# Performance work log

Hardware: AMD Instinct MI355X
Metric: run time of the kernel (lower is better)

Reference implementation:

```python
import jax, jax.numpy as jnp
import numpy as np
from jax import lax

P = 0.1  # WTA keep fraction (mode='per_image')


def setup_inputs() -> dict:
    key = jax.random.key(0)
    x = jax.random.normal(key, (32, 256, 64, 64), dtype=jnp.float32)
    return {"x": x}


def reference(x) -> jnp.ndarray:
    bs, nc, sz, _ = x.shape
    k = int(np.ceil(nc * sz * sz * P))  # 104858 for these shapes
    flat = x.reshape(bs, -1)                      # [bs, nc*sz*sz]
    topk_vals = lax.top_k(flat, k)[0]             # [bs, k], descending
    thr = topk_vals[:, -1].reshape(bs, 1, 1, 1)   # k-th largest per image
    return x * (x >= thr).astype(x.dtype)
```

## Files before the change

### kernel.cpp

```cpp
#include <hip/hip_runtime.h>
#include <hip/hip_bf16.h>
#include <stdint.h>


#define IMGS    32
#define NPER    1048576
#define NPER4   (NPER / 4)
#define NBINS   8192
#define BPI_H   32
#define BPI_M   64
#define CAP     16384
#define LCAP    2048
#define CSTRIDE 64

__device__ __forceinline__ unsigned mapf(float f) {
    unsigned u = __float_as_uint(f);
    return (u & 0x80000000u) ? ~u : (u | 0x80000000u);
}

__device__ __forceinline__ void block_scan256(unsigned* p, int t, unsigned v) {
    p[t] = v;
    __syncthreads();
    #pragma unroll
    for (int off = 1; off < 256; off <<= 1) {
        unsigned u = (t >= off) ? p[t - off] : 0u;
        __syncthreads();
        p[t] += u;
        __syncthreads();
    }
}

__global__ void k_zero(uint4* __restrict__ p, int n16) {
    int i = blockIdx.x * blockDim.x + threadIdx.x;
    if (i < n16) p[i] = make_uint4(0u, 0u, 0u, 0u);
}

__global__ void k_hist(const float4* __restrict__ x4, unsigned* __restrict__ hist) {
    __shared__ unsigned h[NBINS];
    int t = threadIdx.x;
    for (int j = t; j < NBINS; j += 256) h[j] = 0u;
    __syncthreads();

    int bx = blockIdx.x;
    int img = bx >> 5;
    long long base4 = (long long)img * NPER4 + (long long)(bx & 31) * 8192;
    for (int it = 0; it < 32; ++it) {
        float4 v = x4[base4 + it * 256 + t];
        atomicAdd(&h[mapf(v.x) >> 19], 1u);
        atomicAdd(&h[mapf(v.y) >> 19], 1u);
        atomicAdd(&h[mapf(v.z) >> 19], 1u);
        atomicAdd(&h[mapf(v.w) >> 19], 1u);
    }
    __syncthreads();

    unsigned* gh = hist + (long long)img * NBINS;
    for (int j = t; j < NBINS; j += 256) {
        unsigned c = h[j];
        if (c) atomicAdd(&gh[j], c);
    }
}

__global__ void k_scan(const unsigned* __restrict__ hist, uint2* __restrict__ binfo,
                       unsigned k) {
    int img = blockIdx.x;
    const unsigned* h = hist + (long long)img * NBINS;
    __shared__ unsigned bins[NBINS];
    __shared__ unsigned pre[256];
    int t = threadIdx.x;

    for (int idx = t; idx < NBINS; idx += 256) bins[idx] = h[idx];
    __syncthreads();

    unsigned s = 0;
    #pragma unroll
    for (int j = 0; j < 32; ++j) s += bins[t * 32 + ((j + t) & 31)];

    block_scan256(pre, t, s);
    unsigned total_above = pre[255] - pre[t];
    if (total_above < k && total_above + s >= k) {
        unsigned cum = total_above;
        for (int j = 31; j >= 0; --j) {
            unsigned v = bins[t * 32 + j];
            cum += v;
            if (cum >= k) {
                binfo[img] = make_uint2((unsigned)(t * 32 + j), k - (cum - v));
                break;
            }
        }
    }
}

__global__ void k_mask(const float4* __restrict__ x4, float4* __restrict__ o4,
                       const uint2* __restrict__ binfo, unsigned* __restrict__ counters,
                       unsigned* __restrict__ candKey, unsigned* __restrict__ candIdx) {
    __shared__ unsigned lkey[LCAP];
    __shared__ unsigned lidx[LCAP];
    __shared__ unsigned lcnt;
    __shared__ unsigned gbase;
    int t = threadIdx.x;
    if (t == 0) lcnt = 0u;
    __syncthreads();

    int bx = blockIdx.x;
    int img = bx >> 6;
    unsigned b13 = binfo[img].x;
    long long base4 = (long long)img * NPER4 + (long long)(bx & 63) * 4096;

    for (int it = 0; it < 16; ++it) {
        long long i = base4 + it * 256 + t;
        float4 v = x4[i];
        unsigned ebase = (unsigned)(i & (NPER4 - 1)) * 4u;
        float4 o;
        float* vp = &v.x;
        float* op = &o.x;
        #pragma unroll
        for (int j = 0; j < 4; ++j) {
            float c = vp[j];
            unsigned key = mapf(c);
            unsigned t13 = key >> 19;
            op[j] = (t13 >= b13) ? c : 0.0f;
            if (t13 == b13) {
                unsigned p = atomicAdd(&lcnt, 1u);
                if (p < LCAP) { lkey[p] = key; lidx[p] = ebase + (unsigned)j; }
            }
        }
        o4[i] = o;
    }
    __syncthreads();

    unsigned n = lcnt;
    if (n > LCAP) n = LCAP;
    if (t == 0) gbase = atomicAdd(&counters[img * CSTRIDE], n);
    __syncthreads();
    unsigned gb = gbase;
    long long cb = (long long)img * CAP;
    for (unsigned j = t; j < n; j += 256u) {
        unsigned pos = gb + j;
        if (pos < CAP) {
            candKey[cb + pos] = lkey[j];
            candIdx[cb + pos] = lidx[j];
        }
    }
}

__global__ void k_select_fix(float* __restrict__ out,
                             const uint2* __restrict__ binfo,
                             const unsigned* __restrict__ counters,
                             const unsigned* __restrict__ candKey,
                             const unsigned* __restrict__ candIdx) {
    int img = blockIdx.x;
    __shared__ unsigned klds[CAP];
    __shared__ unsigned h2[2048];
    __shared__ unsigned h256[256];
    __shared__ unsigned pre[256];
    __shared__ unsigned sh_p11, sh_r2, sh_thr;
    int t = threadIdx.x;

    unsigned cnt = counters[img * CSTRIDE];
    if (cnt > CAP) cnt = CAP;
    unsigned r = binfo[img].y;
    const unsigned* ck = candKey + (long long)img * CAP;
    const unsigned* ci = candIdx + (long long)img * CAP;

    for (int j = t; j < 2048; j += 256) h2[j] = 0u;
    __syncthreads();

    for (unsigned j = t; j < cnt; j += 256u) {
        unsigned kl = ck[j] & 0x7FFFFu;
        klds[j] = kl;
        atomicAdd(&h2[kl >> 8], 1u);
    }
    __syncthreads();

    unsigned s = 0;
    #pragma unroll
    for (int j = 0; j < 8; ++j) s += h2[t * 8 + ((j + t) & 7)];
    block_scan256(pre, t, s);
    unsigned above = pre[255] - pre[t];
    if (above < r && above + s >= r) {
        unsigned cum = above;
        for (int j = 7; j >= 0; --j) {
            unsigned v = h2[t * 8 + j];
            cum += v;
            if (cum >= r) {
                sh_p11 = (unsigned)(t * 8 + j);
                sh_r2 = r - (cum - v);
                break;
            }
        }
    }
    __syncthreads();
    unsigned p11 = sh_p11, r2 = sh_r2;

    h256[t] = 0u;
    __syncthreads();
    for (unsigned j = t; j < cnt; j += 256u) {
        unsigned kl = klds[j];
        if ((kl >> 8) == p11) atomicAdd(&h256[kl & 0xFFu], 1u);
    }
    __syncthreads();
    unsigned v = h256[t];
    block_scan256(pre, t, v);
    unsigned above2 = pre[255] - pre[t];
    if (above2 < r2 && above2 + v >= r2)
        sh_thr = (p11 << 8) | (unsigned)t;
    __syncthreads();
    unsigned thr = sh_thr;

    float* oi = out + (long long)img * NPER;
    for (unsigned j = t; j < cnt; j += 256u) {
        if (klds[j] < thr) oi[ci[j]] = 0.0f;
    }
}

extern "C" void kernel_launch(void* const* d_in, const int* in_sizes, int n_in,
                              void* d_out, int out_size, void* d_ws, size_t ws_size,
                              hipStream_t stream) {
    const float* x = (const float*)d_in[0];
    float* out = (float*)d_out;
    unsigned k = (unsigned)((NPER + 9) / 10);

    char* ws = (char*)d_ws;
    size_t histB = (size_t)IMGS * NBINS * 4;
    size_t cntB  = (size_t)IMGS * CSTRIDE * 4;
    unsigned* hist     = (unsigned*)ws;
    unsigned* counters = (unsigned*)(ws + histB);
    uint2*    binfo    = (uint2*)   (ws + histB + cntB);
    unsigned* candKey  = (unsigned*)(ws + histB + cntB + 1024);
    unsigned* candIdx  = (unsigned*)(ws + histB + cntB + 1024
                                        + (size_t)IMGS * CAP * 4);

    int n16 = (int)((histB + cntB) / 16);
    k_zero<<<dim3((n16 + 255) / 256), dim3(256), 0, stream>>>((uint4*)ws, n16);

    dim3 blk(256);
    k_hist<<<dim3(IMGS * BPI_H), blk, 0, stream>>>((const float4*)x, hist);
    k_scan<<<dim3(IMGS), blk, 0, stream>>>(hist, binfo, k);
    k_mask<<<dim3(IMGS * BPI_M), blk, 0, stream>>>((const float4*)x, (float4*)out,
                                                   binfo, counters, candKey, candIdx);
    k_select_fix<<<dim3(IMGS), blk, 0, stream>>>(out, binfo, counters, candKey, candIdx);
}
```

Before: 114.2 us.

## Fuse per-image scan and select-fix into producer kernels via last-block tickets

Merges the histogram and scan kernels, and the mask and select-fix kernels, using a per-image atomic ticket. The last block to finish for each image runs the follow-up stage. This drops two kernel launches and the gaps between them, and lets tail work for one image overlap with other images still in progress. The shared memory for mask and fix is unioned, and the candidate keys are re-read from global memory instead of being cached in LDS.

Result: slower. 249.8 us (+118.7%).

```diff
diff --git a/kernel.cpp b/kernel.cpp
--- a/kernel.cpp
+++ b/kernel.cpp
@@ -35,8 +35,12 @@
     if (i < n16) p[i] = make_uint4(0u, 0u, 0u, 0u);
 }
 
-__global__ void k_hist(const float4* __restrict__ x4, unsigned* __restrict__ hist) {
+__global__ void k_hist_scan(const float4* __restrict__ x4, unsigned* __restrict__ hist,
+                            unsigned* __restrict__ done0, uint2* __restrict__ binfo,
+                            unsigned k) {
     __shared__ unsigned h[NBINS];
+    __shared__ unsigned pre[256];
+    __shared__ unsigned sticket;
     int t = threadIdx.x;
     for (int j = t; j < NBINS; j += 256) h[j] = 0u;
     __syncthreads();
@@ -58,29 +62,27 @@
         unsigned c = h[j];
         if (c) atomicAdd(&gh[j], c);
     }
-}
-
-__global__ void k_scan(const unsigned* __restrict__ hist, uint2* __restrict__ binfo,
-                       unsigned k) {
-    int img = blockIdx.x;
-    const unsigned* h = hist + (long long)img * NBINS;
-    __shared__ unsigned bins[NBINS];
-    __shared__ unsigned pre[256];
-    int t = threadIdx.x;
-
-    for (int idx = t; idx < NBINS; idx += 256) bins[idx] = h[idx];
+    __syncthreads();
+    if (t == 0) {
+        __threadfence();
+        sticket = atomicAdd(&done0[img * CSTRIDE], 1u);
+    }
+    __syncthreads();
+    if (sticket != BPI_H - 1) return;
+
+    __threadfence();
+    for (int j = t; j < NBINS; j += 256) h[j] = gh[j];
     __syncthreads();
 
     unsigned s = 0;
     #pragma unroll
-    for (int j = 0; j < 32; ++j) s += bins[t * 32 + ((j + t) & 31)];
-
+    for (int j = 0; j < 32; ++j) s += h[t * 32 + ((j + t) & 31)];
     block_scan256(pre, t, s);
-    unsigned total_above = pre[255] - pre[t];
-    if (total_above < k && total_above + s >= k) {
-        unsigned cum = total_above;
+    unsigned above = pre[255] - pre[t];
+    if (above < k && above + s >= k) {
+        unsigned cum = above;
         for (int j = 31; j >= 0; --j) {
-            unsigned v = bins[t * 32 + j];
+            unsigned v = h[t * 32 + j];
             cum += v;
             if (cum >= k) {
                 binfo[img] = make_uint2((unsigned)(t * 32 + j), k - (cum - v));
@@ -90,13 +92,16 @@
     }
 }
 
-__global__ void k_mask(const float4* __restrict__ x4, float4* __restrict__ o4,
-                       const uint2* __restrict__ binfo, unsigned* __restrict__ counters,
-                       unsigned* __restrict__ candKey, unsigned* __restrict__ candIdx) {
-    __shared__ unsigned lkey[LCAP];
-    __shared__ unsigned lidx[LCAP];
-    __shared__ unsigned lcnt;
-    __shared__ unsigned gbase;
+__global__ void k_mask_fix(const float4* __restrict__ x4, float4* __restrict__ o4,
+                           const uint2* __restrict__ binfo,
+                           unsigned* __restrict__ counters, unsigned* __restrict__ done1,
+                           unsigned* __restrict__ candKey, unsigned* __restrict__ candIdx) {
+    __shared__ union {
+        struct { unsigned lkey[LCAP]; unsigned lidx[LCAP]; } m;
+        struct { unsigned h2[2048]; unsigned h256[256]; unsigned pre[256]; } f;
+    } u;
+    __shared__ unsigned lcnt, gbase, sticket;
+    __shared__ unsigned sh_p11, sh_r2, sh_thr;
     int t = threadIdx.x;
     if (t == 0) lcnt = 0u;
     __syncthreads();
@@ -121,7 +126,7 @@
             op[j] = (t13 >= b13) ? c : 0.0f;
             if (t13 == b13) {
                 unsigned p = atomicAdd(&lcnt, 1u);
-                if (p < LCAP) { lkey[p] = key; lidx[p] = ebase + (unsigned)j; }
+                if (p < LCAP) { u.m.lkey[p] = key; u.m.lidx[p] = ebase + (unsigned)j; }
             }
         }
         o4[i] = o;
@@ -137,50 +142,40 @@
     for (unsigned j = t; j < n; j += 256u) {
         unsigned pos = gb + j;
         if (pos < CAP) {
-            candKey[cb + pos] = lkey[j];
-            candIdx[cb + pos] = lidx[j];
-        }
-    }
-}
-
-__global__ void k_select_fix(float* __restrict__ out,
-                             const uint2* __restrict__ binfo,
-                             const unsigned* __restrict__ counters,
-                             const unsigned* __restrict__ candKey,
-                             const unsigned* __restrict__ candIdx) {
-    int img = blockIdx.x;
-    __shared__ unsigned klds[CAP];
-    __shared__ unsigned h2[2048];
-    __shared__ unsigned h256[256];
-    __shared__ unsigned pre[256];
-    __shared__ unsigned sh_p11, sh_r2, sh_thr;
-    int t = threadIdx.x;
-
+            candKey[cb + pos] = u.m.lkey[j];
+            candIdx[cb + pos] = u.m.lidx[j];
+        }
+    }
+    __syncthreads();
+    if (t == 0) {
+        __threadfence();
+        sticket = atomicAdd(&done1[img * CSTRIDE], 1u);
+    }
+    __syncthreads();
+    if (sticket != BPI_M - 1) return;
+
+    __threadfence();
     unsigned cnt = counters[img * CSTRIDE];
     if (cnt > CAP) cnt = CAP;
     unsigned r = binfo[img].y;
-    const unsigned* ck = candKey + (long long)img * CAP;
-    const unsigned* ci = candIdx + (long long)img * CAP;
-
-    for (int j = t; j < 2048; j += 256) h2[j] = 0u;
-    __syncthreads();
-
-    for (unsigned j = t; j < cnt; j += 256u) {
-        unsigned kl = ck[j] & 0x7FFFFu;
-        klds[j] = kl;
-        atomicAdd(&h2[kl >> 8], 1u);
-    }
+    const unsigned* ck = candKey + cb;
+    const unsigned* ci = candIdx + cb;
+
+    for (int j = t; j < 2048; j += 256) u.f.h2[j] = 0u;
+    __syncthreads();
+    for (unsigned j = t; j < cnt; j += 256u)
+        atomicAdd(&u.f.h2[(ck[j] & 0x7FFFFu) >> 8], 1u);
     __syncthreads();
 
     unsigned s = 0;
     #pragma unroll
-    for (int j = 0; j < 8; ++j) s += h2[t * 8 + ((j + t) & 7)];
-    block_scan256(pre, t, s);
-    unsigned above = pre[255] - pre[t];
+    for (int j = 0; j < 8; ++j) s += u.f.h2[t * 8 + ((j + t) & 7)];
+    block_scan256(u.f.pre, t, s);
+    unsigned above = u.f.pre[255] - u.f.pre[t];
     if (above < r && above + s >= r) {
         unsigned cum = above;
         for (int j = 7; j >= 0; --j) {
-            unsigned v = h2[t * 8 + j];
+            unsigned v = u.f.h2[t * 8 + j];
             cum += v;
             if (cum >= r) {
                 sh_p11 = (unsigned)(t * 8 + j);
@@ -192,24 +187,24 @@
     __syncthreads();
     unsigned p11 = sh_p11, r2 = sh_r2;
 
-    h256[t] = 0u;
+    u.f.h256[t] = 0u;
     __syncthreads();
     for (unsigned j = t; j < cnt; j += 256u) {
-        unsigned kl = klds[j];
-        if ((kl >> 8) == p11) atomicAdd(&h256[kl & 0xFFu], 1u);
-    }
-    __syncthreads();
-    unsigned v = h256[t];
-    block_scan256(pre, t, v);
-    unsigned above2 = pre[255] - pre[t];
+        unsigned kl = ck[j] & 0x7FFFFu;
+        if ((kl >> 8) == p11) atomicAdd(&u.f.h256[kl & 0xFFu], 1u);
+    }
+    __syncthreads();
+    unsigned v = u.f.h256[t];
+    block_scan256(u.f.pre, t, v);
+    unsigned above2 = u.f.pre[255] - u.f.pre[t];
     if (above2 < r2 && above2 + v >= r2)
         sh_thr = (p11 << 8) | (unsigned)t;
     __syncthreads();
     unsigned thr = sh_thr;
 
-    float* oi = out + (long long)img * NPER;
+    float* oi = (float*)o4 + (long long)img * NPER;
     for (unsigned j = t; j < cnt; j += 256u) {
-        if (klds[j] < thr) oi[ci[j]] = 0.0f;
+        if ((ck[j] & 0x7FFFFu) < thr) oi[ci[j]] = 0.0f;
     }
 }
 
@@ -222,21 +217,23 @@
 
     char* ws = (char*)d_ws;
     size_t histB = (size_t)IMGS * NBINS * 4;
-    size_t cntB  = (size_t)IMGS * CSTRIDE * 4;
+    size_t padB  = (size_t)IMGS * CSTRIDE * 4;
     unsigned* hist     = (unsigned*)ws;
     unsigned* counters = (unsigned*)(ws + histB);
-    uint2*    binfo    = (uint2*)   (ws + histB + cntB);
-    unsigned* candKey  = (unsigned*)(ws + histB + cntB + 1024);
-    unsigned* candIdx  = (unsigned*)(ws + histB + cntB + 1024
+    unsigned* done0    = (unsigned*)(ws + histB + padB);
+    unsigned* done1    = (unsigned*)(ws + histB + 2 * padB);
+    uint2*    binfo    = (uint2*)   (ws + histB + 3 * padB);
+    unsigned* candKey  = (unsigned*)(ws + histB + 3 * padB + 1024);
+    unsigned* candIdx  = (unsigned*)(ws + histB + 3 * padB + 1024
                                         + (size_t)IMGS * CAP * 4);
 
-    int n16 = (int)((histB + cntB) / 16);
+    int n16 = (int)((histB + 3 * padB) / 16);
     k_zero<<<dim3((n16 + 255) / 256), dim3(256), 0, stream>>>((uint4*)ws, n16);
 
     dim3 blk(256);
-    k_hist<<<dim3(IMGS * BPI_H), blk, 0, stream>>>((const float4*)x, hist);
-    k_scan<<<dim3(IMGS), blk, 0, stream>>>(hist, binfo, k);
-    k_mask<<<dim3(IMGS * BPI_M), blk, 0, stream>>>((const float4*)x, (float4*)out,
-                                                   binfo, counters, candKey, candIdx);
-    k_select_fix<<<dim3(IMGS), blk, 0, stream>>>(out, binfo, counters, candKey, candIdx);
-}
+    k_hist_scan<<<dim3(IMGS * BPI_H), blk, 0, stream>>>((const float4*)x, hist,
+                                                        done0, binfo, k);
+    k_mask_fix<<<dim3(IMGS * BPI_M), blk, 0, stream>>>((const float4*)x, (float4*)out,
+                                                       binfo, counters, done1,
+                                                       candKey, candIdx);
+}
```

## Replace full histogram pass with sampled window plus exact candidate select

Applied to the files above, without the earlier changes.

The full-image histogram pass and its zeroing kernel are replaced with a per-image sample histogram that reads 1/16 of the elements and brackets the k-th value inside a safety window. A counting pass then tallies elements above the window and collects in-window keys, a three-round radix select finds the exact threshold, and a final masking pass writes the output with nontemporal stores. This removes the post-hoc scattered fixup and the index buffer, at the cost of reading the input twice in full. It also relies on the true threshold falling inside the sampled window; if it does not, or if the LCAP/CAPC candidate buffers overflow, the result will be wrong.

After: 278.4 us. +143.8%, slower.

```diff
diff --git a/kernel.cpp b/kernel.cpp
--- a/kernel.cpp
+++ b/kernel.cpp
@@ -7,11 +7,13 @@
 #define NPER    1048576
 #define NPER4   (NPER / 4)
 #define NBINS   8192
-#define BPI_H   32
-#define BPI_M   64
-#define CAP     16384
+#define BPI     64
+#define MARGIN  32768u
+#define CAPC    98304
 #define LCAP    2048
 #define CSTRIDE 64
+
+typedef float floatx4 __attribute__((ext_vector_type(4)));
 
 __device__ __forceinline__ unsigned mapf(float f) {
     unsigned u = __float_as_uint(f);
@@ -30,22 +32,20 @@
     }
 }
 
-__global__ void k_zero(uint4* __restrict__ p, int n16) {
-    int i = blockIdx.x * blockDim.x + threadIdx.x;
-    if (i < n16) p[i] = make_uint4(0u, 0u, 0u, 0u);
-}
-
-__global__ void k_hist(const float4* __restrict__ x4, unsigned* __restrict__ hist) {
+__global__ void k_sample(const float4* __restrict__ x4, uint2* __restrict__ win,
+                         unsigned* __restrict__ cnt_hi, unsigned* __restrict__ candCnt,
+                         unsigned k) {
     __shared__ unsigned h[NBINS];
-    int t = threadIdx.x;
+    __shared__ unsigned pre[256];
+    __shared__ unsigned s_hi, s_lo;
+    int t = threadIdx.x, img = blockIdx.x;
+    if (t == 0) { cnt_hi[img * CSTRIDE] = 0u; candCnt[img * CSTRIDE] = 0u; }
     for (int j = t; j < NBINS; j += 256) h[j] = 0u;
     __syncthreads();
 
-    int bx = blockIdx.x;
-    int img = bx >> 5;
-    long long base4 = (long long)img * NPER4 + (long long)(bx & 31) * 8192;
-    for (int it = 0; it < 32; ++it) {
-        float4 v = x4[base4 + it * 256 + t];
+    long long ib = (long long)img * NPER4;
+    for (int c = 0; c < 64; ++c) {
+        float4 v = x4[ib + (long long)c * 4096 + t];
         atomicAdd(&h[mapf(v.x) >> 19], 1u);
         atomicAdd(&h[mapf(v.y) >> 19], 1u);
         atomicAdd(&h[mapf(v.z) >> 19], 1u);
@@ -53,163 +53,160 @@
     }
     __syncthreads();
 
-    unsigned* gh = hist + (long long)img * NBINS;
-    for (int j = t; j < NBINS; j += 256) {
-        unsigned c = h[j];
-        if (c) atomicAdd(&gh[j], c);
-    }
-}
-
-__global__ void k_scan(const unsigned* __restrict__ hist, uint2* __restrict__ binfo,
-                       unsigned k) {
-    int img = blockIdx.x;
-    const unsigned* h = hist + (long long)img * NBINS;
-    __shared__ unsigned bins[NBINS];
-    __shared__ unsigned pre[256];
-    int t = threadIdx.x;
-
-    for (int idx = t; idx < NBINS; idx += 256) bins[idx] = h[idx];
-    __syncthreads();
-
     unsigned s = 0;
     #pragma unroll
-    for (int j = 0; j < 32; ++j) s += bins[t * 32 + ((j + t) & 31)];
-
+    for (int j = 0; j < 32; ++j) s += h[t * 32 + ((j + t) & 31)];
     block_scan256(pre, t, s);
-    unsigned total_above = pre[255] - pre[t];
-    if (total_above < k && total_above + s >= k) {
-        unsigned cum = total_above;
+    unsigned above = pre[255] - pre[t];
+
+    unsigned tk_hi = (k > MARGIN) ? (k - MARGIN) : 1u;
+    unsigned tk_lo = k + MARGIN;
+    unsigned tgt_hi = (tk_hi + 15u) >> 4;
+    unsigned tgt_lo = (tk_lo + 15u) >> 4;
+
+    if (above < tgt_hi && above + s >= tgt_hi) {
+        unsigned cum = above;
         for (int j = 31; j >= 0; --j) {
-            unsigned v = bins[t * 32 + j];
+            unsigned v = h[t * 32 + j];
             cum += v;
-            if (cum >= k) {
-                binfo[img] = make_uint2((unsigned)(t * 32 + j), k - (cum - v));
-                break;
+            if (cum >= tgt_hi) { s_hi = (unsigned)(t * 32 + j); break; }
+        }
+    }
+    if (above < tgt_lo && above + s >= tgt_lo) {
+        unsigned cum = above;
+        for (int j = 31; j >= 0; --j) {
+            unsigned v = h[t * 32 + j];
+            cum += v;
+            if (cum >= tgt_lo) { s_lo = (unsigned)(t * 32 + j); break; }
+        }
+    }
+    __syncthreads();
+    if (t == 0) {
+        unsigned hi_key = (s_hi >= 8191u) ? 0xFFFFFFFFu : ((s_hi + 1u) << 19);
+        unsigned lo_key = s_lo << 19;
+        win[img] = make_uint2(lo_key, hi_key);
+    }
+}
+
+__global__ void k_count(const float4* __restrict__ x4, const uint2* __restrict__ win,
+                        unsigned* __restrict__ cnt_hi, unsigned* __restrict__ candCnt,
+                        unsigned* __restrict__ candKey) {
+    __shared__ unsigned lkey[LCAP];
+    __shared__ unsigned red[256];
+    __shared__ unsigned lcnt, gbase;
+    int t = threadIdx.x, bx = blockIdx.x, img = bx >> 6;
+    if (t == 0) lcnt = 0u;
+    __syncthreads();
+
+    uint2 w = win[img];
+    unsigned c = 0;
+    long long base4 = (long long)img * NPER4 + (long long)(bx & 63) * 4096;
+    for (int it = 0; it < 16; ++it) {
+        float4 v = x4[base4 + it * 256 + t];
+        float* vp = &v.x;
+        #pragma unroll
+        for (int j = 0; j < 4; ++j) {
+            unsigned key = mapf(vp[j]);
+            c += (key >= w.y) ? 1u : 0u;
+            if (key >= w.x && key < w.y) {
+                unsigned p = atomicAdd(&lcnt, 1u);
+                if (p < LCAP) lkey[p] = key;
             }
         }
     }
+    red[t] = c;
+    __syncthreads();
+    for (int off = 128; off > 0; off >>= 1) {
+        if (t < off) red[t] += red[t + off];
+        __syncthreads();
+    }
+    unsigned n = lcnt;
+    if (n > LCAP) n = LCAP;
+    if (t == 0) {
+        atomicAdd(&cnt_hi[img * CSTRIDE], red[0]);
+        gbase = atomicAdd(&candCnt[img * CSTRIDE], n);
+    }
+    __syncthreads();
+    unsigned gb = gbase;
+    long long cb = (long long)img * CAPC;
+    for (unsigned j = t; j < n; j += 256u) {
+        unsigned pos = gb + j;
+        if (pos < CAPC) candKey[cb + pos] = lkey[j];
+    }
+}
+
+__global__ void k_select(const unsigned* __restrict__ cnt_hi,
+                         const unsigned* __restrict__ candCnt,
+                         const unsigned* __restrict__ candKey,
+                         unsigned* __restrict__ thrArr, unsigned k) {
+    int img = blockIdx.x, t = threadIdx.x;
+    __shared__ unsigned h2[2048];
+    __shared__ unsigned pre[256];
+    __shared__ unsigned sbin, srank;
+
+    unsigned n = candCnt[img * CSTRIDE];
+    if (n > CAPC) n = CAPC;
+    unsigned chi = cnt_hi[img * CSTRIDE];
+    unsigned r = (k > chi) ? (k - chi) : 1u;
+    if (r > n) r = n;
+    const unsigned* ck = candKey + (long long)img * CAPC;
+
+    unsigned pfx = 0u;
+    const int shifts[3]  = {21, 10, 0};
+    const int fshift[3]  = {32, 21, 10};
+    const int nbits[3]   = {11, 11, 10};
+    for (int rd = 0; rd < 3; ++rd) {
+        for (int j = t; j < 2048; j += 256) h2[j] = 0u;
+        __syncthreads();
+        int sh = shifts[rd];
+        unsigned bmask = (1u << nbits[rd]) - 1u;
+        for (unsigned j = t; j < n; j += 256u) {
+            unsigned key = ck[j];
+            bool ok = (rd == 0) || ((key >> fshift[rd]) == pfx);
+            if (ok) atomicAdd(&h2[(key >> sh) & bmask], 1u);
+        }
+        __syncthreads();
+
+        int bpt = (int)((bmask + 1u) >> 8);
+        unsigned s = 0;
+        for (int j = 0; j < bpt; ++j) s += h2[t * bpt + ((j + t) & (bpt - 1))];
+        block_scan256(pre, t, s);
+        unsigned above = pre[255] - pre[t];
+        if (above < r && above + s >= r) {
+            unsigned cum = above;
+            for (int j = bpt - 1; j >= 0; --j) {
+                unsigned v = h2[t * bpt + j];
+                cum += v;
+                if (cum >= r) {
+                    sbin = (unsigned)(t * bpt + j);
+                    srank = r - (cum - v);
+                    break;
+                }
+            }
+        }
+        __syncthreads();
+        pfx = (pfx << nbits[rd]) | sbin;
+        r = srank;
+        __syncthreads();
+    }
+    if (t == 0) thrArr[img] = pfx;
 }
 
 __global__ void k_mask(const float4* __restrict__ x4, float4* __restrict__ o4,
-                       const uint2* __restrict__ binfo, unsigned* __restrict__ counters,
-                       unsigned* __restrict__ candKey, unsigned* __restrict__ candIdx) {
-    __shared__ unsigned lkey[LCAP];
-    __shared__ unsigned lidx[LCAP];
-    __shared__ unsigned lcnt;
-    __shared__ unsigned gbase;
-    int t = threadIdx.x;
-    if (t == 0) lcnt = 0u;
-    __syncthreads();
-
-    int bx = blockIdx.x;
-    int img = bx >> 6;
-    unsigned b13 = binfo[img].x;
+                       const unsigned* __restrict__ thrArr) {
+    int bx = blockIdx.x, t = threadIdx.x, img = bx >> 6;
+    unsigned thr = thrArr[img];
     long long base4 = (long long)img * NPER4 + (long long)(bx & 63) * 4096;
-
     for (int it = 0; it < 16; ++it) {
         long long i = base4 + it * 256 + t;
         float4 v = x4[i];
-        unsigned ebase = (unsigned)(i & (NPER4 - 1)) * 4u;
         float4 o;
-        float* vp = &v.x;
-        float* op = &o.x;
-        #pragma unroll
-        for (int j = 0; j < 4; ++j) {
-            float c = vp[j];
-            unsigned key = mapf(c);
-            unsigned t13 = key >> 19;
-            op[j] = (t13 >= b13) ? c : 0.0f;
-            if (t13 == b13) {
-                unsigned p = atomicAdd(&lcnt, 1u);
-                if (p < LCAP) { lkey[p] = key; lidx[p] = ebase + (unsigned)j; }
-            }
-        }
-        o4[i] = o;
-    }
-    __syncthreads();
-
-    unsigned n = lcnt;
-    if (n > LCAP) n = LCAP;
-    if (t == 0) gbase = atomicAdd(&counters[img * CSTRIDE], n);
-    __syncthreads();
-    unsigned gb = gbase;
-    long long cb = (long long)img * CAP;
-    for (unsigned j = t; j < n; j += 256u) {
-        unsigned pos = gb + j;
-        if (pos < CAP) {
-            candKey[cb + pos] = lkey[j];
-            candIdx[cb + pos] = lidx[j];
-        }
-    }
-}
-
-__global__ void k_select_fix(float* __restrict__ out,
-                             const uint2* __restrict__ binfo,
-                             const unsigned* __restrict__ counters,
-                             const unsigned* __restrict__ candKey,
-                             const unsigned* __restrict__ candIdx) {
-    int img = blockIdx.x;
-    __shared__ unsigned klds[CAP];
-    __shared__ unsigned h2[2048];
-    __shared__ unsigned h256[256];
-    __shared__ unsigned pre[256];
-    __shared__ unsigned sh_p11, sh_r2, sh_thr;
-    int t = threadIdx.x;
-
-    unsigned cnt = counters[img * CSTRIDE];
-    if (cnt > CAP) cnt = CAP;
-    unsigned r = binfo[img].y;
-    const unsigned* ck = candKey + (long long)img * CAP;
-    const unsigned* ci = candIdx + (long long)img * CAP;
-
-    for (int j = t; j < 2048; j += 256) h2[j] = 0u;
-    __syncthreads();
-
-    for (unsigned j = t; j < cnt; j += 256u) {
-        unsigned kl = ck[j] & 0x7FFFFu;
-        klds[j] = kl;
-        atomicAdd(&h2[kl >> 8], 1u);
-    }
-    __syncthreads();
-
-    unsigned s = 0;
-    #pragma unroll
-    for (int j = 0; j < 8; ++j) s += h2[t * 8 + ((j + t) & 7)];
-    block_scan256(pre, t, s);
-    unsigned above = pre[255] - pre[t];
-    if (above < r && above + s >= r) {
-        unsigned cum = above;
-        for (int j = 7; j >= 0; --j) {
-            unsigned v = h2[t * 8 + j];
-            cum += v;
-            if (cum >= r) {
-                sh_p11 = (unsigned)(t * 8 + j);
-                sh_r2 = r - (cum - v);
-                break;
-            }
-        }
-    }
-    __syncthreads();
-    unsigned p11 = sh_p11, r2 = sh_r2;
-
-    h256[t] = 0u;
-    __syncthreads();
-    for (unsigned j = t; j < cnt; j += 256u) {
-        unsigned kl = klds[j];
-        if ((kl >> 8) == p11) atomicAdd(&h256[kl & 0xFFu], 1u);
-    }
-    __syncthreads();
-    unsigned v = h256[t];
-    block_scan256(pre, t, v);
-    unsigned above2 = pre[255] - pre[t];
-    if (above2 < r2 && above2 + v >= r2)
-        sh_thr = (p11 << 8) | (unsigned)t;
-    __syncthreads();
-    unsigned thr = sh_thr;
-
-    float* oi = out + (long long)img * NPER;
-    for (unsigned j = t; j < cnt; j += 256u) {
-        if (klds[j] < thr) oi[ci[j]] = 0.0f;
+        o.x = (mapf(v.x) >= thr) ? v.x : 0.0f;
+        o.y = (mapf(v.y) >= thr) ? v.y : 0.0f;
+        o.z = (mapf(v.z) >= thr) ? v.z : 0.0f;
+        o.w = (mapf(v.w) >= thr) ? v.w : 0.0f;
+        floatx4 ov = { o.x, o.y, o.z, o.w };
+        __builtin_nontemporal_store(ov, (floatx4*)&o4[i]);
     }
 }
 
@@ -221,22 +218,17 @@
     unsigned k = (unsigned)((NPER + 9) / 10);
 
     char* ws = (char*)d_ws;
-    size_t histB = (size_t)IMGS * NBINS * 4;
-    size_t cntB  = (size_t)IMGS * CSTRIDE * 4;
-    unsigned* hist     = (unsigned*)ws;
-    unsigned* counters = (unsigned*)(ws + histB);
-    uint2*    binfo    = (uint2*)   (ws + histB + cntB);
-    unsigned* candKey  = (unsigned*)(ws + histB + cntB + 1024);
-    unsigned* candIdx  = (unsigned*)(ws + histB + cntB + 1024
-                                        + (size_t)IMGS * CAP * 4);
-
-    int n16 = (int)((histB + cntB) / 16);
-    k_zero<<<dim3((n16 + 255) / 256), dim3(256), 0, stream>>>((uint4*)ws, n16);
+    size_t padB = (size_t)IMGS * CSTRIDE * 4;
+    unsigned* cnt_hi  = (unsigned*)ws;
+    unsigned* candCnt = (unsigned*)(ws + padB);
+    uint2*    win     = (uint2*)   (ws + 2 * padB);
+    unsigned* thrArr  = (unsigned*)(ws + 2 * padB + 1024);
+    unsigned* candKey = (unsigned*)(ws + 2 * padB + 2048);
 
     dim3 blk(256);
-    k_hist<<<dim3(IMGS * BPI_H), blk, 0, stream>>>((const float4*)x, hist);
-    k_scan<<<dim3(IMGS), blk, 0, stream>>>(hist, binfo, k);
-    k_mask<<<dim3(IMGS * BPI_M), blk, 0, stream>>>((const float4*)x, (float4*)out,
-                                                   binfo, counters, candKey, candIdx);
-    k_select_fix<<<dim3(IMGS), blk, 0, stream>>>(out, binfo, counters, candKey, candIdx);
-}
+    k_sample<<<dim3(IMGS), blk, 0, stream>>>((const float4*)x, win, cnt_hi, candCnt, k);
+    k_count<<<dim3(IMGS * BPI), blk, 0, stream>>>((const float4*)x, win,
+                                                  cnt_hi, candCnt, candKey);
+    k_select<<<dim3(IMGS), blk, 0, stream>>>(cnt_hi, candCnt, candKey, thrArr, k);
+    k_mask<<<dim3(IMGS * BPI), blk, 0, stream>>>((const float4*)x, (float4*)out, thrArr);
+}
```
